# Performance work log

Hardware: AMD Instinct MI355X
Metric: run time of the kernel (lower is better)

## Reference

```python
import jax, jax.numpy as jnp
import numpy as np

N_NODES = 50000
N_EDGES = 800000
HID = 128

def _silu(x):
    return x * jax.nn.sigmoid(x)

def setup_inputs() -> dict:
    key = jax.random.key(0)
    ks = jax.random.split(key, 8)
    s = lambda fan_in: 1.0 / np.sqrt(fan_in)
    return {
        "h": jax.random.normal(ks[0], (N_NODES, HID), jnp.float32),
        "edges": jax.random.randint(ks[1], (2, N_EDGES), 0, N_NODES, jnp.int64),
        "distances": jax.random.uniform(ks[2], (N_EDGES, 1), jnp.float32),
        "W_e1": jax.random.normal(ks[3], (2 * HID + 1, HID), jnp.float32) * s(2 * HID + 1),
        "b_e1": jnp.zeros((HID,), jnp.float32),
        "W_e2": jax.random.normal(ks[4], (HID, HID), jnp.float32) * s(HID),
        "b_e2": jnp.zeros((HID,), jnp.float32),
        "W_ei": jax.random.normal(ks[5], (HID, 1), jnp.float32) * s(HID),
        "b_ei": jnp.zeros((1,), jnp.float32),
        "W_n1": jax.random.normal(ks[6], (HID + 1, HID), jnp.float32) * s(HID + 1),
        "b_n1": jnp.zeros((HID,), jnp.float32),
        "W_n2": jax.random.normal(ks[7], (HID, HID), jnp.float32) * s(HID),
        "b_n2": jnp.zeros((HID,), jnp.float32),
    }

def reference(h, edges, distances, W_e1, b_e1, W_e2, b_e2, W_ei, b_ei, W_n1, b_n1, W_n2, b_n2):
    row, col = edges[0], edges[1]
    # edge MLP + sigmoid gate (computed as in original; output unused downstream)
    einp = jnp.concatenate([h[row], h[col], distances], axis=1)   # [E, 2H+1]
    m = _silu(einp @ W_e1 + b_e1)
    m = _silu(m @ W_e2 + b_e2)
    edge_feat = jax.nn.sigmoid(m @ W_ei + b_ei) * m               # [E, H]
    del edge_feat  # original forward never consumes it
    # scatter-add of distances into per-node aggregate, scaled by 1/100
    agg = jax.ops.segment_sum(distances, row, num_segments=h.shape[0]) / 100.0  # [N, 1]
    # node update MLP with residual
    ninp = jnp.concatenate([h, agg], axis=-1)                      # [N, H+1]
    u = _silu(ninp @ W_n1 + b_n1) @ W_n2 + b_n2
    return h + u
```

## Files before the change

### kernel.cpp

```cpp
#include <hip/hip_runtime.h>

#define HID 128
#define NODE_PAD 50048
#define NRANGE 4
#define RANGE 12512
#define NPART 64
#define NGRP 8

typedef __attribute__((ext_vector_type(8))) short short8;
typedef __attribute__((ext_vector_type(4))) float floatx4;

__device__ __forceinline__ short f2bf(float f) {
    unsigned u = __builtin_bit_cast(unsigned, f);
    unsigned r = (u + 0x7FFFu + ((u >> 16) & 1u)) >> 16;
    return (short)r;
}

__global__ __launch_bounds__(256) void scatter_lds(const int* __restrict__ rows,
                                                   const float* __restrict__ dist,
                                                   float* __restrict__ part,
                                                   int n_edges) {
    __shared__ float bins[RANGE];
    const int r = blockIdx.x & (NRANGE - 1);
    const int b = blockIdx.x >> 2;
    const int base = r * RANGE;

    for (int i = threadIdx.x; i < RANGE / 4; i += 256)
        ((float4*)bins)[i] = make_float4(0.f, 0.f, 0.f, 0.f);
    __syncthreads();

    const int chunk = (n_edges + NPART - 1) / NPART;
    const int cbeg = b * chunk;
    const int cend = min(cbeg + chunk, n_edges);

    for (int i = cbeg + threadIdx.x * 4; i < cend; i += 256 * 4) {
        if (i + 4 <= cend) {
            int4   rr = *(const int4*)(rows + i);
            float4 dd = *(const float4*)(dist + i);
            if ((unsigned)(rr.x - base) < RANGE) atomicAdd(&bins[rr.x - base], dd.x);
            if ((unsigned)(rr.y - base) < RANGE) atomicAdd(&bins[rr.y - base], dd.y);
            if ((unsigned)(rr.z - base) < RANGE) atomicAdd(&bins[rr.z - base], dd.z);
            if ((unsigned)(rr.w - base) < RANGE) atomicAdd(&bins[rr.w - base], dd.w);
        } else {
            for (int j = i; j < cend; ++j) {
                int rw = rows[j];
                if ((unsigned)(rw - base) < RANGE) atomicAdd(&bins[rw - base], dist[j]);
            }
        }
    }
    __syncthreads();

    float4* dst = (float4*)(part + (size_t)b * NODE_PAD + base);
    for (int i = threadIdx.x; i < RANGE / 4; i += 256)
        dst[i] = ((const float4*)bins)[i];
}

__global__ __launch_bounds__(256) void reduce_partials(const float* __restrict__ part,
                                                       float* __restrict__ agg8) {
    const int g   = blockIdx.x & (NGRP - 1);
    const int blk = blockIdx.x >> 3;
    const int i   = blk * 256 + threadIdx.x;
    const int nc4 = NODE_PAD / 4;
    if (i < nc4) {
        const float4* p = (const float4*)part + (size_t)g * (NPART / NGRP) * nc4 + i;
        float4 s = make_float4(0.f, 0.f, 0.f, 0.f);
#pragma unroll
        for (int c = 0; c < NPART / NGRP; ++c) {
            float4 v = p[(size_t)c * nc4];
            s.x += v.x; s.y += v.y; s.z += v.z; s.w += v.w;
        }
        ((float4*)agg8)[(size_t)g * nc4 + i] = s;
    }
}

__global__ void convert_weights(const float* __restrict__ W1,
                                const float* __restrict__ W2,
                                short* __restrict__ W1t,
                                short* __restrict__ W2t) {
    int t = blockIdx.x * blockDim.x + threadIdx.x;
    int idx = t & 16383;
    int n = idx & 127, k = idx >> 7;
    if (t < 16384) W1t[n * 128 + k] = f2bf(W1[k * 128 + n]);
    else           W2t[n * 128 + k] = f2bf(W2[k * 128 + n]);
}

__global__ __launch_bounds__(512) void node_mlp_mfma(
    const float* __restrict__ h,
    const float* __restrict__ agg8,
    const short* __restrict__ W1t,
    const short* __restrict__ W2t,
    const float* __restrict__ W1,
    const float* __restrict__ b1,
    const float* __restrict__ b2,
    float* __restrict__ out,
    int n_nodes)
{
    __shared__ short WL[128 * 136];
    __shared__ short t_lds[8][16 * 136];

    const int tid  = threadIdx.x;
    const int wv   = tid >> 6;
    const int lane = tid & 63;
    const int m16  = lane & 15;
    const int quad = lane >> 4;
    const int node0 = blockIdx.x * 128 + wv * 16;

    short8 a1[4];
    {
        int row = node0 + m16;
        if (row >= n_nodes) row = n_nodes - 1;
        const float* hr = h + (size_t)row * HID + quad * 8;
#pragma unroll
        for (int kc = 0; kc < 4; ++kc) {
            float4 x0 = *(const float4*)(hr + kc * 32);
            float4 x1 = *(const float4*)(hr + kc * 32 + 4);
            short8 v;
            v[0] = f2bf(x0.x); v[1] = f2bf(x0.y); v[2] = f2bf(x0.z); v[3] = f2bf(x0.w);
            v[4] = f2bf(x1.x); v[5] = f2bf(x1.y); v[6] = f2bf(x1.z); v[7] = f2bf(x1.w);
            a1[kc] = v;
        }
    }

    float4 a4;
    {
        float4 s = make_float4(0.f, 0.f, 0.f, 0.f);
#pragma unroll
        for (int g = 0; g < NGRP; ++g) {
            float4 p = *(const float4*)(agg8 + (size_t)g * NODE_PAD + node0 + quad * 4);
            s.x += p.x; s.y += p.y; s.z += p.z; s.w += p.w;
        }
        a4.x = s.x * 0.01f; a4.y = s.y * 0.01f; a4.z = s.z * 0.01f; a4.w = s.w * 0.01f;
    }

#pragma unroll
    for (int i = 0; i < 4; ++i) {
        int idx = tid + i * 512;
        int n = idx >> 4, c = idx & 15;
        *(float4*)(WL + n * 136 + c * 8) = ((const float4*)W1t)[idx];
    }
    __syncthreads();

#pragma unroll
    for (int nt = 0; nt < 8; ++nt) {
        floatx4 acc = {0.f, 0.f, 0.f, 0.f};
        const short* wb = WL + (nt * 16 + m16) * 136 + quad * 8;
#pragma unroll
        for (int kc = 0; kc < 4; ++kc) {
            short8 bfr = *(const short8*)(wb + kc * 32);
            acc = __builtin_amdgcn_mfma_f32_16x16x32_bf16(a1[kc], bfr, acc, 0, 0, 0);
        }
        int col = nt * 16 + m16;
        float bias = b1[col];
        float wagg = W1[128 * HID + col];
        float av[4] = {a4.x, a4.y, a4.z, a4.w};
#pragma unroll
        for (int r = 0; r < 4; ++r) {
            float v = acc[r] + bias + av[r] * wagg;
            float sg = __builtin_amdgcn_rcpf(1.0f + __expf(-v));
            v *= sg;
            t_lds[wv][(quad * 4 + r) * 136 + col] = f2bf(v);
        }
    }

    __syncthreads();

#pragma unroll
    for (int i = 0; i < 4; ++i) {
        int idx = tid + i * 512;
        int n = idx >> 4, c = idx & 15;
        *(float4*)(WL + n * 136 + c * 8) = ((const float4*)W2t)[idx];
    }
    __syncthreads();

    short8 a2[4];
#pragma unroll
    for (int kc = 0; kc < 4; ++kc)
        a2[kc] = *(const short8*)(&t_lds[wv][m16 * 136 + kc * 32 + quad * 8]);

#pragma unroll
    for (int nt = 0; nt < 8; ++nt) {
        floatx4 acc = {0.f, 0.f, 0.f, 0.f};
        const short* wb = WL + (nt * 16 + m16) * 136 + quad * 8;
#pragma unroll
        for (int kc = 0; kc < 4; ++kc) {
            short8 bfr = *(const short8*)(wb + kc * 32);
            acc = __builtin_amdgcn_mfma_f32_16x16x32_bf16(a2[kc], bfr, acc, 0, 0, 0);
        }
        int col = nt * 16 + m16;
        float bias = b2[col];
#pragma unroll
        for (int r = 0; r < 4; ++r) {
            int row = node0 + quad * 4 + r;
            if (row < n_nodes) {
                size_t off = (size_t)row * HID + col;
                out[off] = h[off] + acc[r] + bias;
            }
        }
    }
}

extern "C" void kernel_launch(void* const* d_in, const int* in_sizes, int n_in,
                              void* d_out, int out_size, void* d_ws, size_t ws_size,
                              hipStream_t stream) {
    const float* h     = (const float*)d_in[0];
    const int*   edges = (const int*)d_in[1];
    const float* dist  = (const float*)d_in[2];
    const float* W1    = (const float*)d_in[9];
    const float* b1    = (const float*)d_in[10];
    const float* W2    = (const float*)d_in[11];
    const float* b2    = (const float*)d_in[12];
    float* out = (float*)d_out;

    const int n_nodes = in_sizes[0] / HID;
    const int n_edges = in_sizes[2];
    const int* rows = edges;

    float* part = (float*)d_ws;
    float* agg8 = part + (size_t)NPART * NODE_PAD;
    short* W1t  = (short*)(agg8 + (size_t)NGRP * NODE_PAD);
    short* W2t  = W1t + 16384;

    convert_weights<<<128, 256, 0, stream>>>(W1, W2, W1t, W2t);

    scatter_lds<<<NRANGE * NPART, 256, 0, stream>>>(rows, dist, part, n_edges);

    reduce_partials<<<NGRP * ((NODE_PAD / 4 + 255) / 256), 256, 0, stream>>>(part, agg8);

    const int blocks = (n_nodes + 127) / 128;
    node_mlp_mfma<<<blocks, 512, 0, stream>>>(h, agg8, W1t, W2t, W1, b1, b2, out,
                                              n_nodes);
}
```

Baseline: 132.1 us.

## Make node MLP persistent with in-block weight conversion and prefetch

Removes the separate weight-conversion kernel: each block now converts and transposes W1 and W2 to bf16 directly into two LDS buffers, once per block. The node MLP becomes a persistent kernel with 256 blocks, where each wave loops over 16-node tiles and prefetches the next tile's h and aggregate values into registers while computing the current one. The partial-reduction group count drops from 8 to 4, so the MLP sums fewer aggregate slices. The aim is to cut launch count, avoid reloading weights per 128-node block, and hide global load latency, at the cost of more LDS and register pressure per block.

```diff
diff --git a/kernel.cpp b/kernel.cpp
--- a/kernel.cpp
+++ b/kernel.cpp
@@ -5,7 +5,7 @@
 #define NRANGE 4
 #define RANGE 12512
 #define NPART 64
-#define NGRP 8
+#define NGRP 4
 
 typedef __attribute__((ext_vector_type(8))) short short8;
 typedef __attribute__((ext_vector_type(4))) float floatx4;
@@ -56,9 +56,9 @@
 }
 
 __global__ __launch_bounds__(256) void reduce_partials(const float* __restrict__ part,
-                                                       float* __restrict__ agg8) {
+                                                       float* __restrict__ agg4) {
     const int g   = blockIdx.x & (NGRP - 1);
-    const int blk = blockIdx.x >> 3;
+    const int blk = blockIdx.x >> 2;
     const int i   = blk * 256 + threadIdx.x;
     const int nc4 = NODE_PAD / 4;
     if (i < nc4) {
@@ -69,33 +69,22 @@
             float4 v = p[(size_t)c * nc4];
             s.x += v.x; s.y += v.y; s.z += v.z; s.w += v.w;
         }
-        ((float4*)agg8)[(size_t)g * nc4 + i] = s;
-    }
-}
-
-__global__ void convert_weights(const float* __restrict__ W1,
-                                const float* __restrict__ W2,
-                                short* __restrict__ W1t,
-                                short* __restrict__ W2t) {
-    int t = blockIdx.x * blockDim.x + threadIdx.x;
-    int idx = t & 16383;
-    int n = idx & 127, k = idx >> 7;
-    if (t < 16384) W1t[n * 128 + k] = f2bf(W1[k * 128 + n]);
-    else           W2t[n * 128 + k] = f2bf(W2[k * 128 + n]);
-}
-
-__global__ __launch_bounds__(512) void node_mlp_mfma(
+        ((float4*)agg4)[(size_t)g * nc4 + i] = s;
+    }
+}
+
+__global__ __launch_bounds__(512, 2) void node_mlp_mfma(
     const float* __restrict__ h,
-    const float* __restrict__ agg8,
-    const short* __restrict__ W1t,
-    const short* __restrict__ W2t,
+    const float* __restrict__ agg4,
     const float* __restrict__ W1,
     const float* __restrict__ b1,
+    const float* __restrict__ W2,
     const float* __restrict__ b2,
     float* __restrict__ out,
-    int n_nodes)
+    int n_nodes, int n_tiles)
 {
-    __shared__ short WL[128 * 136];
+    __shared__ short WL1[128 * 136];
+    __shared__ short WL2[128 * 136];
     __shared__ short t_lds[8][16 * 136];
 
     const int tid  = threadIdx.x;
@@ -103,99 +92,141 @@
     const int lane = tid & 63;
     const int m16  = lane & 15;
     const int quad = lane >> 4;
-    const int node0 = blockIdx.x * 128 + wv * 16;
-
-    short8 a1[4];
+
     {
-        int row = node0 + m16;
+        const int kg = tid >> 5;
+        const int c  = tid & 31;
+        const float* s1 = W1 + (size_t)(kg * 8) * HID + c * 4;
+        const float* s2 = W2 + (size_t)(kg * 8) * HID + c * 4;
+        float r1[8][4], r2[8][4];
+#pragma unroll
+        for (int j = 0; j < 8; ++j) {
+            *(float4*)r1[j] = *(const float4*)(s1 + j * HID);
+            *(float4*)r2[j] = *(const float4*)(s2 + j * HID);
+        }
+#pragma unroll
+        for (int jj = 0; jj < 4; ++jj) {
+            short8 v1, v2;
+#pragma unroll
+            for (int j = 0; j < 8; ++j) {
+                v1[j] = f2bf(r1[j][jj]);
+                v2[j] = f2bf(r2[j][jj]);
+            }
+            *(short8*)(WL1 + (c * 4 + jj) * 136 + kg * 8) = v1;
+            *(short8*)(WL2 + (c * 4 + jj) * 136 + kg * 8) = v2;
+        }
+    }
+
+    float b1v[8], b2v[8], wgv[8];
+#pragma unroll
+    for (int nt = 0; nt < 8; ++nt) {
+        int col = nt * 16 + m16;
+        b1v[nt] = b1[col];
+        b2v[nt] = b2[col];
+        wgv[nt] = W1[(size_t)HID * HID + col];
+    }
+
+    __syncthreads();
+
+    const int tstride = gridDim.x * 8;
+    int tile = blockIdx.x * 8 + wv;
+
+    float4 hb[8];
+    float4 ab[NGRP];
+    if (tile < n_tiles) {
+        int row = tile * 16 + m16;
         if (row >= n_nodes) row = n_nodes - 1;
         const float* hr = h + (size_t)row * HID + quad * 8;
 #pragma unroll
         for (int kc = 0; kc < 4; ++kc) {
-            float4 x0 = *(const float4*)(hr + kc * 32);
-            float4 x1 = *(const float4*)(hr + kc * 32 + 4);
+            hb[2 * kc]     = *(const float4*)(hr + kc * 32);
+            hb[2 * kc + 1] = *(const float4*)(hr + kc * 32 + 4);
+        }
+#pragma unroll
+        for (int g = 0; g < NGRP; ++g)
+            ab[g] = *(const float4*)(agg4 + (size_t)g * NODE_PAD + tile * 16 + quad * 4);
+    }
+
+    while (tile < n_tiles) {
+        const int node0 = tile * 16;
+
+        short8 a1[4];
+#pragma unroll
+        for (int kc = 0; kc < 4; ++kc) {
             short8 v;
-            v[0] = f2bf(x0.x); v[1] = f2bf(x0.y); v[2] = f2bf(x0.z); v[3] = f2bf(x0.w);
-            v[4] = f2bf(x1.x); v[5] = f2bf(x1.y); v[6] = f2bf(x1.z); v[7] = f2bf(x1.w);
+            v[0] = f2bf(hb[2 * kc].x);     v[1] = f2bf(hb[2 * kc].y);
+            v[2] = f2bf(hb[2 * kc].z);     v[3] = f2bf(hb[2 * kc].w);
+            v[4] = f2bf(hb[2 * kc + 1].x); v[5] = f2bf(hb[2 * kc + 1].y);
+            v[6] = f2bf(hb[2 * kc + 1].z); v[7] = f2bf(hb[2 * kc + 1].w);
             a1[kc] = v;
         }
-    }
-
-    float4 a4;
-    {
-        float4 s = make_float4(0.f, 0.f, 0.f, 0.f);
-#pragma unroll
-        for (int g = 0; g < NGRP; ++g) {
-            float4 p = *(const float4*)(agg8 + (size_t)g * NODE_PAD + node0 + quad * 4);
-            s.x += p.x; s.y += p.y; s.z += p.z; s.w += p.w;
-        }
-        a4.x = s.x * 0.01f; a4.y = s.y * 0.01f; a4.z = s.z * 0.01f; a4.w = s.w * 0.01f;
-    }
-
-#pragma unroll
-    for (int i = 0; i < 4; ++i) {
-        int idx = tid + i * 512;
-        int n = idx >> 4, c = idx & 15;
-        *(float4*)(WL + n * 136 + c * 8) = ((const float4*)W1t)[idx];
-    }
-    __syncthreads();
-
-#pragma unroll
-    for (int nt = 0; nt < 8; ++nt) {
-        floatx4 acc = {0.f, 0.f, 0.f, 0.f};
-        const short* wb = WL + (nt * 16 + m16) * 136 + quad * 8;
-#pragma unroll
-        for (int kc = 0; kc < 4; ++kc) {
-            short8 bfr = *(const short8*)(wb + kc * 32);
-            acc = __builtin_amdgcn_mfma_f32_16x16x32_bf16(a1[kc], bfr, acc, 0, 0, 0);
-        }
-        int col = nt * 16 + m16;
-        float bias = b1[col];
-        float wagg = W1[128 * HID + col];
-        float av[4] = {a4.x, a4.y, a4.z, a4.w};
-#pragma unroll
-        for (int r = 0; r < 4; ++r) {
-            float v = acc[r] + bias + av[r] * wagg;
-            float sg = __builtin_amdgcn_rcpf(1.0f + __expf(-v));
-            v *= sg;
-            t_lds[wv][(quad * 4 + r) * 136 + col] = f2bf(v);
-        }
-    }
-
-    __syncthreads();
-
-#pragma unroll
-    for (int i = 0; i < 4; ++i) {
-        int idx = tid + i * 512;
-        int n = idx >> 4, c = idx & 15;
-        *(float4*)(WL + n * 136 + c * 8) = ((const float4*)W2t)[idx];
-    }
-    __syncthreads();
-
-    short8 a2[4];
-#pragma unroll
-    for (int kc = 0; kc < 4; ++kc)
-        a2[kc] = *(const short8*)(&t_lds[wv][m16 * 136 + kc * 32 + quad * 8]);
-
-#pragma unroll
-    for (int nt = 0; nt < 8; ++nt) {
-        floatx4 acc = {0.f, 0.f, 0.f, 0.f};
-        const short* wb = WL + (nt * 16 + m16) * 136 + quad * 8;
-#pragma unroll
-        for (int kc = 0; kc < 4; ++kc) {
-            short8 bfr = *(const short8*)(wb + kc * 32);
-            acc = __builtin_amdgcn_mfma_f32_16x16x32_bf16(a2[kc], bfr, acc, 0, 0, 0);
-        }
-        int col = nt * 16 + m16;
-        float bias = b2[col];
-#pragma unroll
-        for (int r = 0; r < 4; ++r) {
-            int row = node0 + quad * 4 + r;
-            if (row < n_nodes) {
-                size_t off = (size_t)row * HID + col;
-                out[off] = h[off] + acc[r] + bias;
-            }
-        }
+        float4 a4;
+        a4.x = (ab[0].x + ab[1].x + ab[2].x + ab[3].x) * 0.01f;
+        a4.y = (ab[0].y + ab[1].y + ab[2].y + ab[3].y) * 0.01f;
+        a4.z = (ab[0].z + ab[1].z + ab[2].z + ab[3].z) * 0.01f;
+        a4.w = (ab[0].w + ab[1].w + ab[2].w + ab[3].w) * 0.01f;
+
+        const int ntile = tile + tstride;
+        if (ntile < n_tiles) {
+            int row = ntile * 16 + m16;
+            if (row >= n_nodes) row = n_nodes - 1;
+            const float* hr = h + (size_t)row * HID + quad * 8;
+#pragma unroll
+            for (int kc = 0; kc < 4; ++kc) {
+                hb[2 * kc]     = *(const float4*)(hr + kc * 32);
+                hb[2 * kc + 1] = *(const float4*)(hr + kc * 32 + 4);
+            }
+#pragma unroll
+            for (int g = 0; g < NGRP; ++g)
+                ab[g] = *(const float4*)(agg4 + (size_t)g * NODE_PAD + ntile * 16 + quad * 4);
+        }
+
+#pragma unroll
+        for (int nt = 0; nt < 8; ++nt) {
+            floatx4 acc = {0.f, 0.f, 0.f, 0.f};
+            const short* wb = WL1 + (nt * 16 + m16) * 136 + quad * 8;
+#pragma unroll
+            for (int kc = 0; kc < 4; ++kc) {
+                short8 bfr = *(const short8*)(wb + kc * 32);
+                acc = __builtin_amdgcn_mfma_f32_16x16x32_bf16(a1[kc], bfr, acc, 0, 0, 0);
+            }
+            int col = nt * 16 + m16;
+            float av[4] = {a4.x, a4.y, a4.z, a4.w};
+#pragma unroll
+            for (int r = 0; r < 4; ++r) {
+                float v = acc[r] + b1v[nt] + av[r] * wgv[nt];
+                float sg = __builtin_amdgcn_rcpf(1.0f + __expf(-v));
+                v *= sg;
+                t_lds[wv][(quad * 4 + r) * 136 + col] = f2bf(v);
+            }
+        }
+
+        short8 a2[4];
+#pragma unroll
+        for (int kc = 0; kc < 4; ++kc)
+            a2[kc] = *(const short8*)(&t_lds[wv][m16 * 136 + kc * 32 + quad * 8]);
+
+#pragma unroll
+        for (int nt = 0; nt < 8; ++nt) {
+            floatx4 acc = {0.f, 0.f, 0.f, 0.f};
+            const short* wb = WL2 + (nt * 16 + m16) * 136 + quad * 8;
+#pragma unroll
+            for (int kc = 0; kc < 4; ++kc) {
+                short8 bfr = *(const short8*)(wb + kc * 32);
+                acc = __builtin_amdgcn_mfma_f32_16x16x32_bf16(a2[kc], bfr, acc, 0, 0, 0);
+            }
+            int col = nt * 16 + m16;
+#pragma unroll
+            for (int r = 0; r < 4; ++r) {
+                int row = node0 + quad * 4 + r;
+                if (row < n_nodes) {
+                    size_t off = (size_t)row * HID + col;
+                    out[off] = h[off] + acc[r] + b2v[nt];
+                }
+            }
+        }
+
+        tile = ntile;
     }
 }
 
@@ -216,17 +247,13 @@
     const int* rows = edges;
 
     float* part = (float*)d_ws;
-    float* agg8 = part + (size_t)NPART * NODE_PAD;
-    short* W1t  = (short*)(agg8 + (size_t)NGRP * NODE_PAD);
-    short* W2t  = W1t + 16384;
-
-    convert_weights<<<128, 256, 0, stream>>>(W1, W2, W1t, W2t);
+    float* agg4 = part + (size_t)NPART * NODE_PAD;
 
     scatter_lds<<<NRANGE * NPART, 256, 0, stream>>>(rows, dist, part, n_edges);
 
-    reduce_partials<<<NGRP * ((NODE_PAD / 4 + 255) / 256), 256, 0, stream>>>(part, agg8);
-
-    const int blocks = (n_nodes + 127) / 128;
-    node_mlp_mfma<<<blocks, 512, 0, stream>>>(h, agg8, W1t, W2t, W1, b1, b2, out,
-                                              n_nodes);
-}
+    reduce_partials<<<NGRP * ((NODE_PAD / 4 + 255) / 256), 256, 0, stream>>>(part, agg4);
+
+    const int n_tiles = (n_nodes + 15) / 16;
+    node_mlp_mfma<<<256, 512, 0, stream>>>(h, agg4, W1, b1, W2, b2, out,
+                                           n_nodes, n_tiles);
+}
```

Result: slower. 139.7 us (+5.7%).
